# Kernel optimization log

Hardware: AMD Instinct MI355X
Metric: run time of the kernel (lower is better)

## Reference

```python
import jax, jax.numpy as jnp
import numpy as np

EPS = 1e-05


def _rms_norm(x, w):
    xf = x.astype(jnp.float32)
    o = xf * jax.lax.rsqrt(jnp.square(xf).mean(-1, keepdims=True) + EPS)
    return (o * w.astype(jnp.float32)).astype(x.dtype)


def _apply_rope(x, sin, cos):
    # x: [B,T,N,H]; sin/cos: [B,T,H/2]
    half = x.shape[-1] // 2
    x1, x2 = x[..., :half], x[..., half:]
    s, c = sin[:, :, None, :], cos[:, :, None, :]
    return jnp.concatenate([x1 * c - x2 * s, x2 * c + x1 * s], axis=-1).astype(x.dtype)


def setup_inputs() -> dict:
    key = jax.random.key(0)
    ks = jax.random.split(key, 12)
    B, T, D, FF, HALF = 2, 1024, 4096, 12288, 64
    return {
        "x": jax.random.normal(ks[0], (B, T, D), jnp.float32),
        "sin": jax.random.uniform(ks[1], (B, T, HALF), jnp.float32),
        "cos": jax.random.uniform(ks[2], (B, T, HALF), jnp.float32),
        "attn_norm_w": jax.random.uniform(ks[3], (D,), jnp.float32),
        "ff_norm_w": jax.random.uniform(ks[4], (D,), jnp.float32),
        "wq": jax.random.normal(ks[5], (D, D), jnp.float32) * 0.02,
        "wk": jax.random.normal(ks[6], (D, D), jnp.float32) * 0.02,
        "wv": jax.random.normal(ks[7], (D, D), jnp.float32) * 0.02,
        "wo": jax.random.normal(ks[8], (D, D), jnp.float32) * 0.02,
        "w_ff": jax.random.normal(ks[9], (D, FF), jnp.float32) * 0.02,
        "w_up": jax.random.normal(ks[10], (D, FF), jnp.float32) * 0.02,
        "w_out": jax.random.normal(ks[11], (FF, D), jnp.float32) * 0.02,
    }


def reference(x, sin, cos, attn_norm_w, ff_norm_w, wq, wk, wv, wo, w_ff, w_up, w_out):
    B, T, D = x.shape
    head_dim = sin.shape[-1] * 2  # 128
    # --- attention ---
    xn = _rms_norm(x, attn_norm_w)
    q = (xn @ wq).reshape(B, T, -1, head_dim)
    k = (xn @ wk).reshape(B, T, -1, head_dim)
    v = (xn @ wv).reshape(B, T, -1, head_dim)
    q = _apply_rope(q, sin, cos)
    k = _apply_rope(k, sin, cos)
    scale = jnp.asarray(1.0 / np.sqrt(head_dim), dtype=q.dtype)
    logits = jnp.einsum("BTNH,BSNH->BNTS", q, k) * scale
    probs = jax.nn.softmax(logits.astype(jnp.float32), axis=-1).astype(k.dtype)
    attn = jnp.einsum("BNTS,BSNH->BTNH", probs, v).reshape(B, T, D)
    x = x + attn @ wo
    # --- SwiGLU MLP ---
    res = x
    xn = _rms_norm(x, ff_norm_w)
    h = jax.nn.silu(xn @ w_ff) * (xn @ w_up)
    return res + h @ w_out
```

## Files before the change

kernel.cpp:

```cpp
#include <hip/hip_runtime.h>


#define D_MODEL 4096
#define FF_DIM  12288
#define SEQ     1024
#define NBATCH  2
#define M_ROWS  2048
#define NHEAD   32
#define HDIM    128
#define QKV_N   12288
#define FF2_N   24576

typedef short bf16x8 __attribute__((ext_vector_type(8)));
typedef float f32x4  __attribute__((ext_vector_type(4)));

__device__ __forceinline__ ushort f2bf(float f) {
  unsigned u = __float_as_uint(f);
  u += 0x7FFFu + ((u >> 16) & 1u);
  return (ushort)(u >> 16);
}
__device__ __forceinline__ float bf2f(ushort u) {
  return __uint_as_float(((unsigned)u) << 16);
}

__device__ __forceinline__ void gload_lds16(const ushort* gsrc, ushort* ldst) {
  __builtin_amdgcn_global_load_lds((const __attribute__((address_space(1))) void*)gsrc,
                                   (__attribute__((address_space(3))) void*)ldst, 16, 0, 0);
}

#define SBAR()  asm volatile("s_barrier" ::: "memory")
#define LGKM0() asm volatile("s_waitcnt lgkmcnt(0)" ::: "memory")
#define VMCNT6() asm volatile("s_waitcnt vmcnt(6)" ::: "memory")

__global__ __launch_bounds__(256)
void transpose_convert(const float* __restrict__ W, ushort* __restrict__ Wt,
                       int K, int N)
{
  __shared__ float tile[32][33];
  const int x = threadIdx.x, y = threadIdx.y;
  const size_t k0 = (size_t)blockIdx.y * 32, n0 = (size_t)blockIdx.x * 32;
#pragma unroll
  for (int i = 0; i < 32; i += 8)
    tile[y + i][x] = W[(k0 + y + i) * N + n0 + x];
  __syncthreads();
#pragma unroll
  for (int i = 0; i < 32; i += 8)
    Wt[(n0 + y + i) * K + k0 + x] = f2bf(tile[x][y + i]);
}

__global__ __launch_bounds__(256)
void rmsnorm_kernel(const float* __restrict__ x, const float* __restrict__ w,
                    ushort* __restrict__ out)
{
  const int row = blockIdx.x, t = threadIdx.x;
  const float* xr = x + (size_t)row * D_MODEL;
  float4 vv[4];
  float ss = 0.f;
#pragma unroll
  for (int p = 0; p < 4; p++) {
    vv[p] = *(const float4*)&xr[p * 1024 + t * 4];
    ss += vv[p].x * vv[p].x + vv[p].y * vv[p].y + vv[p].z * vv[p].z + vv[p].w * vv[p].w;
  }
#pragma unroll
  for (int mm = 1; mm < 64; mm <<= 1) ss += __shfl_xor(ss, mm);
  __shared__ float wsum[4];
  if ((t & 63) == 0) wsum[t >> 6] = ss;
  __syncthreads();
  ss = wsum[0] + wsum[1] + wsum[2] + wsum[3];
  const float rs = rsqrtf(ss * (1.f / 4096.f) + 1e-5f);
#pragma unroll
  for (int p = 0; p < 4; p++) {
    const float4 wv = *(const float4*)&w[p * 1024 + t * 4];
    ushort4 ov;
    ov.x = f2bf(vv[p].x * rs * wv.x);
    ov.y = f2bf(vv[p].y * rs * wv.y);
    ov.z = f2bf(vv[p].z * rs * wv.z);
    ov.w = f2bf(vv[p].w * rs * wv.w);
    *(ushort4*)&out[(size_t)row * D_MODEL + p * 1024 + t * 4] = ov;
  }
}

__global__ __launch_bounds__(256)
void rope_kernel(ushort* __restrict__ q, ushort* __restrict__ k,
                 const float* __restrict__ sinp, const float* __restrict__ cosp,
                 int ld)
{
  const size_t idx = (size_t)blockIdx.x * 256 + threadIdx.x;
  const int d = (int)(idx & 63);
  const int h = (int)((idx >> 6) & 31);
  const int t = (int)(idx >> 11);
  const float s = sinp[t * 64 + d], c = cosp[t * 64 + d];
  const size_t base = (size_t)t * ld + h * HDIM + d;
  const float q1 = bf2f(q[base]), q2 = bf2f(q[base + 64]);
  q[base]      = f2bf(q1 * c - q2 * s);
  q[base + 64] = f2bf(q2 * c + q1 * s);
  const float k1 = bf2f(k[base]), k2 = bf2f(k[base + 64]);
  k[base]      = f2bf(k1 * c - k2 * s);
  k[base + 64] = f2bf(k2 * c + k1 * s);
}

__global__ __launch_bounds__(64)
void attn_fwd(const ushort* __restrict__ q, const ushort* __restrict__ k,
              const ushort* __restrict__ v, ushort* __restrict__ o,
              int ldq, int ldo)
{
  const int l = threadIdx.x, c16 = l & 15, g = l >> 4;
  const int qt = blockIdx.x, h = blockIdx.y, b = blockIdx.z;
  __shared__ __align__(16) ushort P_lds[16 * 32];

  const size_t head_off = (size_t)h * HDIM;
  const size_t rowQ = (size_t)(b * SEQ + qt * 16 + c16);
  bf16x8 qf[4];
#pragma unroll
  for (int kc = 0; kc < 4; kc++)
    qf[kc] = *(const bf16x8*)(q + rowQ * ldq + head_off + kc * 32 + g * 8);

  f32x4 oacc[8];
#pragma unroll
  for (int i = 0; i < 8; i++) oacc[i] = (f32x4){0.f, 0.f, 0.f, 0.f};
  float mrow[4] = {-1e30f, -1e30f, -1e30f, -1e30f};
  float lrow[4] = {0.f, 0.f, 0.f, 0.f};
  const float scale = 0.08838834764831845f;
  const float L2E = 1.4426950408889634f;

  for (int s0 = 0; s0 < SEQ; s0 += 32) {
    f32x4 st[2];
#pragma unroll
    for (int t = 0; t < 2; t++) {
      f32x4 a = (f32x4){0.f, 0.f, 0.f, 0.f};
      const ushort* kb = k + (size_t)(b * SEQ + s0 + t * 16 + c16) * ldq + head_off + g * 8;
#pragma unroll
      for (int kc = 0; kc < 4; kc++) {
        bf16x8 kf = *(const bf16x8*)(kb + kc * 32);
        a = __builtin_amdgcn_mfma_f32_16x16x32_bf16(qf[kc], kf, a, 0, 0, 0);
      }
      st[t] = a;
    }
#pragma unroll
    for (int r = 0; r < 4; r++) {
      const float s0v = st[0][r] * scale, s1v = st[1][r] * scale;
      float cm = fmaxf(s0v, s1v);
#pragma unroll
      for (int mm = 1; mm < 16; mm <<= 1) cm = fmaxf(cm, __shfl_xor(cm, mm));
      const float mn = fmaxf(mrow[r], cm);
      const float alpha = exp2f((mrow[r] - mn) * L2E);
      const float p0 = exp2f((s0v - mn) * L2E);
      const float p1 = exp2f((s1v - mn) * L2E);
      float rsum = p0 + p1;
#pragma unroll
      for (int mm = 1; mm < 16; mm <<= 1) rsum += __shfl_xor(rsum, mm);
      lrow[r] = lrow[r] * alpha + rsum;
      mrow[r] = mn;
#pragma unroll
      for (int dbi = 0; dbi < 8; dbi++) oacc[dbi] *= alpha;
      P_lds[(g * 4 + r) * 32 + c16]      = f2bf(p0);
      P_lds[(g * 4 + r) * 32 + 16 + c16] = f2bf(p1);
    }
    __syncthreads();
    const bf16x8 pf = *(const bf16x8*)&P_lds[c16 * 32 + g * 8];
#pragma unroll
    for (int dbi = 0; dbi < 8; dbi++) {
      bf16x8 vf;
      const ushort* vb = v + (size_t)(b * SEQ + s0 + g * 8) * ldq + head_off + dbi * 16 + c16;
#pragma unroll
      for (int j = 0; j < 8; j++) vf[j] = (short)vb[(size_t)j * ldq];
      oacc[dbi] = __builtin_amdgcn_mfma_f32_16x16x32_bf16(pf, vf, oacc[dbi], 0, 0, 0);
    }
    __syncthreads();
  }
  const size_t rowO = (size_t)(b * SEQ + qt * 16 + g * 4);
#pragma unroll
  for (int dbi = 0; dbi < 8; dbi++)
#pragma unroll
    for (int r = 0; r < 4; r++)
      o[(rowO + r) * ldo + head_off + dbi * 16 + c16] = f2bf(oacc[dbi][r] / lrow[r]);
}

__global__ __launch_bounds__(256)
void swiglu_kernel(const ushort* __restrict__ hraw, ushort* __restrict__ g)
{
  const int m = blockIdx.y;
  const int c = (blockIdx.x * 256 + threadIdx.x) * 8;
  const ushort* hp = hraw + (size_t)m * FF2_N + c;
  bf16x8 hv = *(const bf16x8*)hp;
  bf16x8 uv = *(const bf16x8*)(hp + FF_DIM);
  bf16x8 ov;
#pragma unroll
  for (int e = 0; e < 8; e++) {
    const float h = bf2f((ushort)hv[e]);
    const float u = bf2f((ushort)uv[e]);
    ov[e] = (short)f2bf((h / (1.f + __expf(-h))) * u);
  }
  *(bf16x8*)(g + (size_t)m * FF_DIM + c) = ov;
}

template <int EPI>
__global__ __launch_bounds__(512, 2)
void gemm8p(const ushort* __restrict__ A, const ushort* __restrict__ Bt,
            const float* __restrict__ res, void* __restrict__ Cout,
            int M, int N, int K)
{
  __shared__ __align__(16) ushort lds[65536];
  const int tid = threadIdx.x;
  const int w = tid >> 6, l = tid & 63;
  const int c16 = l & 15, g = l >> 4;
  const int wr = w >> 2, wc = w & 3;

  const int nx = N >> 8;
  const int nwg = gridDim.x;
  const int q8 = nwg >> 3, r8 = nwg & 7;
  const int xcd = blockIdx.x & 7, loc = blockIdx.x >> 3;
  const int wg = (xcd < r8 ? xcd * (q8 + 1) : r8 * (q8 + 1) + (xcd - r8) * q8) + loc;
  const size_t m0 = (size_t)(wg / nx) * 256;
  const size_t n0 = (size_t)(wg % nx) * 256;
  const int nk = K >> 6;

  const int srow  = (w << 3) + (l >> 3);
  const int scolE = ((l & 7) ^ (l >> 3)) << 3;
  const ushort* gA = A  + (m0 + srow) * (size_t)K + scolE;
  const ushort* gB = Bt + (n0 + srow) * (size_t)K + scolE;

#define STG_A(p, h, q, tk)                                                        \
  gload_lds16(gA + (size_t)((h) * 128 + (q) * 64) * K + (size_t)(tk) * 64,        \
              lds + (p) * 16384 + (h) * 8192 + (q) * 4096 + (w << 9))
#define STG_B(p, h, q, tk)                                                        \
  gload_lds16(gB + (size_t)((h) * 128 + (q) * 64) * K + (size_t)(tk) * 64,        \
              lds + 32768 + (p) * 16384 + (h) * 8192 + (q) * 4096 + (w << 9))
#define STG_A2(p, h, tk) do { STG_A(p, h, 0, tk); STG_A(p, h, 1, tk); } while (0)
#define STG_B2(p, h, tk) do { STG_B(p, h, 0, tk); STG_B(p, h, 1, tk); } while (0)

  const int xorE = (c16 & 7) << 3;
  const int k0E = (g * 8) ^ xorE;
  const int k1E = (32 + g * 8) ^ xorE;
  const int aRow = wr * 64 + c16;
  const int bRow = wc * 32 + c16;

  auto LDA = [&](int p, int qm, int i, int ke) -> bf16x8 {
    return *(const bf16x8*)(lds + p * 16384 + (qm * 128 + aRow + i * 16) * 64 + ke);
  };
  auto LDB = [&](int p, int qn, int j, int ke) -> bf16x8 {
    return *(const bf16x8*)(lds + 32768 + p * 16384 + (qn * 128 + bRow + j * 16) * 64 + ke);
  };

  f32x4 acc[8][4];
#pragma unroll
  for (int i = 0; i < 8; i++)
#pragma unroll
    for (int j = 0; j < 4; j++) acc[i][j] = (f32x4){0.f, 0.f, 0.f, 0.f};
  bf16x8 a[4][2], b0[2][2], b1[2][2];

  STG_A2(0, 0, 0); STG_A2(0, 1, 0); STG_B2(0, 0, 0); STG_B2(0, 1, 0);
  STG_A2(1, 0, 1); STG_B2(1, 0, 1); STG_B2(1, 1, 1);
  VMCNT6(); SBAR();

  for (int t = 0; t < nk; ++t) {
    const int p = t & 1;
    const int tn1 = (t + 1 < nk) ? t + 1 : t + 1 - nk;
    const int tn2 = (t + 2 < nk) ? t + 2 : t + 2 - nk;

#pragma unroll
    for (int i = 0; i < 4; ++i) { a[i][0] = LDA(p, 0, i, k0E); a[i][1] = LDA(p, 0, i, k1E); }
#pragma unroll
    for (int j = 0; j < 2; ++j) { b0[j][0] = LDB(p, 0, j, k0E); b0[j][1] = LDB(p, 0, j, k1E); }
    STG_A2(p ^ 1, 1, tn1);
    SBAR(); LGKM0();
    __builtin_amdgcn_s_setprio(1);
#pragma unroll
    for (int i = 0; i < 4; ++i)
#pragma unroll
      for (int j = 0; j < 2; ++j)
#pragma unroll
        for (int kk = 0; kk < 2; ++kk)
          acc[i][j] = __builtin_amdgcn_mfma_f32_16x16x32_bf16(a[i][kk], b0[j][kk], acc[i][j], 0, 0, 0);
    __builtin_amdgcn_s_setprio(0);
    SBAR();

#pragma unroll
    for (int j = 0; j < 2; ++j) { b1[j][0] = LDB(p, 1, j, k0E); b1[j][1] = LDB(p, 1, j, k1E); }
    STG_A2(p, 0, tn2);
    SBAR(); LGKM0();
    __builtin_amdgcn_s_setprio(1);
#pragma unroll
    for (int i = 0; i < 4; ++i)
#pragma unroll
      for (int j = 0; j < 2; ++j)
#pragma unroll
        for (int kk = 0; kk < 2; ++kk)
          acc[i][2 + j] = __builtin_amdgcn_mfma_f32_16x16x32_bf16(a[i][kk], b1[j][kk], acc[i][2 + j], 0, 0, 0);
    __builtin_amdgcn_s_setprio(0);
    SBAR();

#pragma unroll
    for (int i = 0; i < 4; ++i) { a[i][0] = LDA(p, 1, i, k0E); a[i][1] = LDA(p, 1, i, k1E); }
    STG_B2(p, 0, tn2);
    SBAR(); LGKM0();
    __builtin_amdgcn_s_setprio(1);
#pragma unroll
    for (int i = 0; i < 4; ++i)
#pragma unroll
      for (int j = 0; j < 2; ++j)
#pragma unroll
        for (int kk = 0; kk < 2; ++kk)
          acc[4 + i][j] = __builtin_amdgcn_mfma_f32_16x16x32_bf16(a[i][kk], b0[j][kk], acc[4 + i][j], 0, 0, 0);
    __builtin_amdgcn_s_setprio(0);
    SBAR();

    STG_B2(p, 1, tn2);
    SBAR(); LGKM0();
    __builtin_amdgcn_s_setprio(1);
#pragma unroll
    for (int i = 0; i < 4; ++i)
#pragma unroll
      for (int j = 0; j < 2; ++j)
#pragma unroll
        for (int kk = 0; kk < 2; ++kk)
          acc[4 + i][2 + j] = __builtin_amdgcn_mfma_f32_16x16x32_bf16(a[i][kk], b1[j][kk], acc[4 + i][2 + j], 0, 0, 0);
    __builtin_amdgcn_s_setprio(0);
    VMCNT6(); SBAR();
  }

#pragma unroll
  for (int qm = 0; qm < 2; qm++)
#pragma unroll
    for (int i = 0; i < 4; i++)
#pragma unroll
      for (int qn = 0; qn < 2; qn++)
#pragma unroll
        for (int j = 0; j < 2; j++)
#pragma unroll
          for (int r = 0; r < 4; r++) {
            const size_t row = m0 + qm * 128 + wr * 64 + i * 16 + g * 4 + r;
            const size_t col = n0 + qn * 128 + wc * 32 + j * 16 + c16;
            const size_t idx = row * N + col;
            const float v = acc[qm * 4 + i][qn * 2 + j][r];
            if constexpr (EPI == 0) {
              ((ushort*)Cout)[idx] = f2bf(v);
            } else {
              ((float*)Cout)[idx] = res[idx] + v;
            }
          }
#undef STG_A
#undef STG_B
#undef STG_A2
#undef STG_B2
}

extern "C" void kernel_launch(void* const* d_in, const int* in_sizes, int n_in,
                              void* d_out, int out_size, void* d_ws, size_t ws_size,
                              hipStream_t stream)
{
  const float* x    = (const float*)d_in[0];
  const float* sinp = (const float*)d_in[1];
  const float* cosp = (const float*)d_in[2];
  const float* anw  = (const float*)d_in[3];
  const float* fnw  = (const float*)d_in[4];
  const float* wq   = (const float*)d_in[5];
  const float* wk   = (const float*)d_in[6];
  const float* wv   = (const float*)d_in[7];
  const float* wo   = (const float*)d_in[8];
  const float* wff  = (const float*)d_in[9];
  const float* wup  = (const float*)d_in[10];
  const float* wout = (const float*)d_in[11];
  float* out = (float*)d_out;

  const size_t szDD   = (size_t)D_MODEL * D_MODEL * 2;
  const size_t szDF   = (size_t)D_MODEL * FF_DIM * 2;
  const size_t szAct2 = (size_t)M_ROWS * D_MODEL * 2;
  const size_t szAct4 = (size_t)M_ROWS * D_MODEL * 4;
  const size_t szQKV  = (size_t)M_ROWS * QKV_N * 2;
  const size_t szFF2  = (size_t)M_ROWS * FF2_N * 2;

  char* ws = (char*)d_ws;
  size_t off = 0;
  auto alloc = [&](size_t bytes) -> char* {
    char* p = ws + off;
    off += (bytes + 255) & ~(size_t)255;
    return p;
  };
  ushort* R1    = (ushort*)alloc(szDF);
  ushort* R2    = (ushort*)alloc(2 * szDF);
  ushort* wot   = (ushort*)alloc(szDD);
  ushort* xn    = (ushort*)alloc(szAct2);
  ushort* qkv   = (ushort*)alloc(szQKV);
  ushort* attnb = (ushort*)alloc(szAct2);
  float*  x2    = (float*)alloc(szAct4);
  ushort* ffraw = (ushort*)alloc(szFF2);
  if (off > ws_size) return;

  const dim3 tb(32, 8);
  transpose_convert<<<dim3(D_MODEL / 32, D_MODEL / 32), tb, 0, stream>>>(wq, R1, D_MODEL, D_MODEL);
  transpose_convert<<<dim3(D_MODEL / 32, D_MODEL / 32), tb, 0, stream>>>(wk, R1 + (size_t)D_MODEL * D_MODEL, D_MODEL, D_MODEL);
  transpose_convert<<<dim3(D_MODEL / 32, D_MODEL / 32), tb, 0, stream>>>(wv, R1 + 2 * (size_t)D_MODEL * D_MODEL, D_MODEL, D_MODEL);
  transpose_convert<<<dim3(D_MODEL / 32, D_MODEL / 32), tb, 0, stream>>>(wo, wot, D_MODEL, D_MODEL);
  transpose_convert<<<dim3(FF_DIM / 32, D_MODEL / 32), tb, 0, stream>>>(wff, R2, D_MODEL, FF_DIM);
  transpose_convert<<<dim3(FF_DIM / 32, D_MODEL / 32), tb, 0, stream>>>(wup, R2 + (size_t)FF_DIM * D_MODEL, D_MODEL, FF_DIM);

  rmsnorm_kernel<<<M_ROWS, 256, 0, stream>>>(x, anw, xn);
  gemm8p<0><<<(M_ROWS / 256) * (QKV_N / 256), 512, 0, stream>>>(xn, R1, nullptr, qkv, M_ROWS, QKV_N, D_MODEL);
  transpose_convert<<<dim3(D_MODEL / 32, FF_DIM / 32), tb, 0, stream>>>(wout, R1, FF_DIM, D_MODEL);
  rope_kernel<<<(M_ROWS * NHEAD * 64) / 256, 256, 0, stream>>>(qkv, qkv + D_MODEL, sinp, cosp, QKV_N);
  attn_fwd<<<dim3(SEQ / 16, NHEAD, NBATCH), 64, 0, stream>>>(qkv, qkv + D_MODEL, qkv + 2 * D_MODEL, attnb, QKV_N, D_MODEL);
  gemm8p<1><<<(M_ROWS / 256) * (D_MODEL / 256), 512, 0, stream>>>(attnb, wot, x, x2, M_ROWS, D_MODEL, D_MODEL);

  rmsnorm_kernel<<<M_ROWS, 256, 0, stream>>>(x2, fnw, xn);
  gemm8p<0><<<(M_ROWS / 256) * (FF2_N / 256), 512, 0, stream>>>(xn, R2, nullptr, ffraw, M_ROWS, FF2_N, D_MODEL);
  swiglu_kernel<<<dim3(FF_DIM / 2048, M_ROWS), 256, 0, stream>>>(ffraw, qkv );
  gemm8p<1><<<(M_ROWS / 256) * (D_MODEL / 256), 512, 0, stream>>>(qkv, R1, x2, out, M_ROWS, D_MODEL, FF_DIM);
}
```

Measured before the change: 1.544 ms.

## Pre-transpose V for attention, reorder GEMM tile mapping and prefetch schedule

Result: slower. 1.634 ms (+5.9%).

```diff
diff --git a/kernel.cpp b/kernel.cpp
--- a/kernel.cpp
+++ b/kernel.cpp
@@ -28,9 +28,9 @@
                                    (__attribute__((address_space(3))) void*)ldst, 16, 0, 0);
 }
 
-#define SBAR()  asm volatile("s_barrier" ::: "memory")
-#define LGKM0() asm volatile("s_waitcnt lgkmcnt(0)" ::: "memory")
-#define VMCNT6() asm volatile("s_waitcnt vmcnt(6)" ::: "memory")
+#define SBAR()   asm volatile("s_barrier" ::: "memory")
+#define LGKM0()  asm volatile("s_waitcnt lgkmcnt(0)" ::: "memory")
+#define VMCNT8() asm volatile("s_waitcnt vmcnt(8)" ::: "memory")
 
 __global__ __launch_bounds__(256)
 void transpose_convert(const float* __restrict__ W, ushort* __restrict__ Wt,
@@ -46,6 +46,25 @@
 #pragma unroll
   for (int i = 0; i < 32; i += 8)
     Wt[(n0 + y + i) * K + k0 + x] = f2bf(tile[x][y + i]);
+}
+
+__global__ __launch_bounds__(256)
+void v_transpose(const ushort* __restrict__ v, ushort* __restrict__ vt)
+{
+  __shared__ ushort tile[32][33];
+  const int x = threadIdx.x, y = threadIdx.y;
+  const int row0 = blockIdx.x * 32;
+  const int d0 = blockIdx.y * 32;
+  const int h = blockIdx.z;
+  const int b = row0 >> 10, sl0 = row0 & (SEQ - 1);
+#pragma unroll
+  for (int i = 0; i < 32; i += 8)
+    tile[y + i][x] = v[(size_t)(row0 + y + i) * QKV_N + h * HDIM + d0 + x];
+  __syncthreads();
+  ushort* ob = vt + ((size_t)(b * NHEAD + h) * HDIM + d0) * SEQ + sl0;
+#pragma unroll
+  for (int i = 0; i < 32; i += 8)
+    ob[(size_t)(y + i) * SEQ + x] = tile[x][y + i];
 }
 
 __global__ __launch_bounds__(256)
@@ -101,7 +120,7 @@
 
 __global__ __launch_bounds__(64)
 void attn_fwd(const ushort* __restrict__ q, const ushort* __restrict__ k,
-              const ushort* __restrict__ v, ushort* __restrict__ o,
+              const ushort* __restrict__ vt, ushort* __restrict__ o,
               int ldq, int ldo)
 {
   const int l = threadIdx.x, c16 = l & 15, g = l >> 4;
@@ -110,6 +129,7 @@
 
   const size_t head_off = (size_t)h * HDIM;
   const size_t rowQ = (size_t)(b * SEQ + qt * 16 + c16);
+  const ushort* vtb = vt + (size_t)(b * NHEAD + h) * HDIM * SEQ;
   bf16x8 qf[4];
 #pragma unroll
   for (int kc = 0; kc < 4; kc++)
@@ -160,10 +180,7 @@
     const bf16x8 pf = *(const bf16x8*)&P_lds[c16 * 32 + g * 8];
 #pragma unroll
     for (int dbi = 0; dbi < 8; dbi++) {
-      bf16x8 vf;
-      const ushort* vb = v + (size_t)(b * SEQ + s0 + g * 8) * ldq + head_off + dbi * 16 + c16;
-#pragma unroll
-      for (int j = 0; j < 8; j++) vf[j] = (short)vb[(size_t)j * ldq];
+      const bf16x8 vf = *(const bf16x8*)(vtb + (size_t)(dbi * 16 + c16) * SEQ + s0 + g * 8);
       oacc[dbi] = __builtin_amdgcn_mfma_f32_16x16x32_bf16(pf, vf, oacc[dbi], 0, 0, 0);
     }
     __syncthreads();
@@ -206,13 +223,12 @@
   const int c16 = l & 15, g = l >> 4;
   const int wr = w >> 2, wc = w & 3;
 
-  const int nx = N >> 8;
   const int nwg = gridDim.x;
   const int q8 = nwg >> 3, r8 = nwg & 7;
   const int xcd = blockIdx.x & 7, loc = blockIdx.x >> 3;
   const int wg = (xcd < r8 ? xcd * (q8 + 1) : r8 * (q8 + 1) + (xcd - r8) * q8) + loc;
-  const size_t m0 = (size_t)(wg / nx) * 256;
-  const size_t n0 = (size_t)(wg % nx) * 256;
+  const size_t m0 = (size_t)(wg & 7) * 256;
+  const size_t n0 = (size_t)(wg >> 3) * 256;
   const int nk = K >> 6;
 
   const int srow  = (w << 3) + (l >> 3);
@@ -250,19 +266,17 @@
   bf16x8 a[4][2], b0[2][2], b1[2][2];
 
   STG_A2(0, 0, 0); STG_A2(0, 1, 0); STG_B2(0, 0, 0); STG_B2(0, 1, 0);
-  STG_A2(1, 0, 1); STG_B2(1, 0, 1); STG_B2(1, 1, 1);
-  VMCNT6(); SBAR();
+  STG_A2(1, 0, 1); STG_A2(1, 1, 1); STG_B2(1, 0, 1); STG_B2(1, 1, 1);
+  VMCNT8(); SBAR();
 
   for (int t = 0; t < nk; ++t) {
     const int p = t & 1;
-    const int tn1 = (t + 1 < nk) ? t + 1 : t + 1 - nk;
     const int tn2 = (t + 2 < nk) ? t + 2 : t + 2 - nk;
 
 #pragma unroll
     for (int i = 0; i < 4; ++i) { a[i][0] = LDA(p, 0, i, k0E); a[i][1] = LDA(p, 0, i, k1E); }
 #pragma unroll
     for (int j = 0; j < 2; ++j) { b0[j][0] = LDB(p, 0, j, k0E); b0[j][1] = LDB(p, 0, j, k1E); }
-    STG_A2(p ^ 1, 1, tn1);
     SBAR(); LGKM0();
     __builtin_amdgcn_s_setprio(1);
 #pragma unroll
@@ -278,6 +292,7 @@
 #pragma unroll
     for (int j = 0; j < 2; ++j) { b1[j][0] = LDB(p, 1, j, k0E); b1[j][1] = LDB(p, 1, j, k1E); }
     STG_A2(p, 0, tn2);
+    STG_B2(p, 0, tn2);
     SBAR(); LGKM0();
     __builtin_amdgcn_s_setprio(1);
 #pragma unroll
@@ -292,7 +307,7 @@
 
 #pragma unroll
     for (int i = 0; i < 4; ++i) { a[i][0] = LDA(p, 1, i, k0E); a[i][1] = LDA(p, 1, i, k1E); }
-    STG_B2(p, 0, tn2);
+    STG_B2(p, 1, tn2);
     SBAR(); LGKM0();
     __builtin_amdgcn_s_setprio(1);
 #pragma unroll
@@ -305,7 +320,7 @@
     __builtin_amdgcn_s_setprio(0);
     SBAR();
 
-    STG_B2(p, 1, tn2);
+    STG_A2(p, 1, tn2);
     SBAR(); LGKM0();
     __builtin_amdgcn_s_setprio(1);
 #pragma unroll
@@ -316,7 +331,7 @@
         for (int kk = 0; kk < 2; ++kk)
           acc[4 + i][2 + j] = __builtin_amdgcn_mfma_f32_16x16x32_bf16(a[i][kk], b1[j][kk], acc[4 + i][2 + j], 0, 0, 0);
     __builtin_amdgcn_s_setprio(0);
-    VMCNT6(); SBAR();
+    VMCNT8(); SBAR();
   }
 
 #pragma unroll
@@ -385,6 +400,7 @@
   ushort* attnb = (ushort*)alloc(szAct2);
   float*  x2    = (float*)alloc(szAct4);
   ushort* ffraw = (ushort*)alloc(szFF2);
+  ushort* vtb   = (ushort*)alloc(szAct2);
   if (off > ws_size) return;
 
   const dim3 tb(32, 8);
@@ -399,7 +415,8 @@
   gemm8p<0><<<(M_ROWS / 256) * (QKV_N / 256), 512, 0, stream>>>(xn, R1, nullptr, qkv, M_ROWS, QKV_N, D_MODEL);
   transpose_convert<<<dim3(D_MODEL / 32, FF_DIM / 32), tb, 0, stream>>>(wout, R1, FF_DIM, D_MODEL);
   rope_kernel<<<(M_ROWS * NHEAD * 64) / 256, 256, 0, stream>>>(qkv, qkv + D_MODEL, sinp, cosp, QKV_N);
-  attn_fwd<<<dim3(SEQ / 16, NHEAD, NBATCH), 64, 0, stream>>>(qkv, qkv + D_MODEL, qkv + 2 * D_MODEL, attnb, QKV_N, D_MODEL);
+  v_transpose<<<dim3(M_ROWS / 32, HDIM / 32, NHEAD), tb, 0, stream>>>(qkv + 2 * D_MODEL, vtb);
+  attn_fwd<<<dim3(SEQ / 16, NHEAD, NBATCH), 64, 0, stream>>>(qkv, qkv + D_MODEL, vtb, attnb, QKV_N, D_MODEL);
   gemm8p<1><<<(M_ROWS / 256) * (D_MODEL / 256), 512, 0, stream>>>(attnb, wot, x, x2, M_ROWS, D_MODEL, D_MODEL);
 
   rmsnorm_kernel<<<M_ROWS, 256, 0, stream>>>(x2, fnw, xn);
```
